# Kernel optimization log

Hardware: AMD Instinct MI355X
Metric: run time of the kernel (lower is better)

Reference implementation:

```python
import jax, jax.numpy as jnp
import numpy as np

B, N, D, E = 2, 50000, 64, 800000


def setup_inputs() -> dict:
    key = jax.random.key(0)
    k = jax.random.split(key, 6)
    return {
        "prev_embeddings": jax.random.normal(k[0], (B, N, D), dtype=jnp.float32),
        "edges_ij": jax.random.randint(k[1], (E, 2), 0, N, dtype=jnp.int64 if jax.config.jax_enable_x64 else jnp.int32),
        "node_features_embeddings": jax.random.normal(k[2], (B, N, D), dtype=jnp.float32),
        "edge_features_embeddings": jax.random.normal(k[3], (B, N, D), dtype=jnp.float32),
        "edge_status": jax.random.uniform(k[4], (E,), dtype=jnp.float32),
        "W": jax.random.normal(k[5], (D, D), dtype=jnp.float32) / np.sqrt(D).astype(np.float32),
    }


def reference(prev_embeddings, edges_ij, node_features_embeddings, edge_features_embeddings, edge_status, W):
    # prev_embeddings: (B, N, D); edges_ij: (E, 2); edge_status: (E,) in [0,1]; W: (D, D) theta2 weight (no bias)
    u = edges_ij[:, 0]
    v = edges_ij[:, 1]
    g = edge_status.astype(prev_embeddings.dtype).reshape(1, -1, 1)  # broadcast (1,E,1) over batch
    h_u = prev_embeddings[:, u, :] * g  # gather source endpoint, gate
    h_v = prev_embeddings[:, v, :] * g  # gather dest endpoint, gate
    # scatter-add gated messages in both directions: nbr[b, v] += h_u, nbr[b, u] += h_v
    nbr = jnp.zeros_like(prev_embeddings).at[:, v, :].add(h_u).at[:, u, :].add(h_v)
    x2 = jnp.einsum('bnd,ed->bne', nbr, W)  # Linear(D,D,bias=False): nbr @ W.T
    return jax.nn.leaky_relu(node_features_embeddings + x2 + edge_features_embeddings)
```

## Files before the change

kernel.cpp:

```cpp
#include <hip/hip_runtime.h>

constexpr int B = 2;
constexpr int N = 50000;
constexpr int D = 64;
constexpr int E = 800000;
constexpr int CAP = 96;
constexpr int XG = 8;
constexpr int NPG = N / XG;
constexpr int CSTRIDE_PAD = 16;

constexpr int ROWS_PER_WAVE = 25;
constexpr int BGROUPS = 1563;
constexpr int PGROUPS = 125;
constexpr int TOTAL_GROUPS = BGROUPS + PGROUPS;

__device__ __forceinline__ unsigned f2bf(float f) {
    unsigned u = __float_as_uint(f);
    return (u + 0x7FFFu + ((u >> 16) & 1u)) >> 16;
}
__device__ __forceinline__ float bfhi2f(unsigned bits) {
    return __uint_as_float(bits & 0xFFFF0000u);
}
__device__ __forceinline__ float bflo2f(unsigned bits) {
    return __uint_as_float(bits << 16);
}

__global__ __launch_bounds__(256) void build_pgemm_fused(
    const int2* __restrict__ edges, const float* __restrict__ status,
    int* __restrict__ counts, unsigned* __restrict__ slots,
    const float* __restrict__ prev, const float* __restrict__ W,
    unsigned* __restrict__ P32, int cstride)
{
    int grp = blockIdx.x >> 3;
    int sub8 = blockIdx.x & 7;
    int t = threadIdx.x;

    int cyc = grp / 13, pos = grp % 13;
    bool is_pgemm = (pos == 12) && (grp < PGROUPS * 13);

    if (!is_pgemm) {
        int b = (grp < PGROUPS * 13) ? (cyc * 12 + pos) : (1500 + (grp - PGROUPS * 13));
        int e0 = b * 512 + t;
        int e1 = e0 + 256;
        bool has1 = (e1 < E);

        int2 uv0 = edges[e0];
        float st0 = status[e0];
        int2 uv1 = has1 ? edges[e1] : uv0;
        float st1 = has1 ? status[e1] : 0.f;
        unsigned gb0 = f2bf(st0) << 16;
        unsigned gb1 = f2bf(st1) << 16;

        bool du0 = (uv0.x / NPG == sub8);
        bool dv0 = (uv0.y / NPG == sub8);
        bool du1 = has1 && (uv1.x / NPG == sub8);
        bool dv1 = has1 && (uv1.y / NPG == sub8);

        int pu0 = CAP, pv0 = CAP, pu1 = CAP, pv1 = CAP;
        if (du0) pu0 = atomicAdd(&counts[(size_t)uv0.x * cstride], 1);
        if (dv0) pv0 = atomicAdd(&counts[(size_t)uv0.y * cstride], 1);
        if (du1) pu1 = atomicAdd(&counts[(size_t)uv1.x * cstride], 1);
        if (dv1) pv1 = atomicAdd(&counts[(size_t)uv1.y * cstride], 1);
        if (du0 && pu0 < CAP) slots[(size_t)uv0.x * CAP + pu0] = gb0 | (unsigned)uv0.y;
        if (dv0 && pv0 < CAP) slots[(size_t)uv0.y * CAP + pv0] = gb0 | (unsigned)uv0.x;
        if (du1 && pu1 < CAP) slots[(size_t)uv1.x * CAP + pu1] = gb1 | (unsigned)uv1.y;
        if (dv1 && pv1 < CAP) slots[(size_t)uv1.y * CAP + pv1] = gb1 | (unsigned)uv1.x;
    } else {
        int pb = cyc * 8 + sub8;
        int wave = t >> 6, lane = t & 63;

        const float4* W4 = (const float4*)W;
        float4 w[16];
#pragma unroll
        for (int q = 0; q < 16; ++q) w[q] = W4[lane * 16 + q];

        int row0 = pb * (4 * ROWS_PER_WAVE) + wave * ROWS_PER_WAVE;
        for (int r = 0; r < ROWS_PER_WAVE; ++r) {
            int row = __builtin_amdgcn_readfirstlane(row0 + r);
            const float* pr = prev + (size_t)row * D;

            float acc = 0.f;
#pragma unroll
            for (int d = 0; d < D; ++d) {
                const float4& wq = w[d >> 2];
                float wd = (d & 3) == 0 ? wq.x : (d & 3) == 1 ? wq.y
                         : (d & 3) == 2 ? wq.z : wq.w;
                acc += pr[d] * wd;
            }

            float partner = __shfl_xor(acc, 1, 64);
            if ((lane & 1) == 0) {
                P32[(size_t)row * 32 + (lane >> 1)] = f2bf(acc) | (f2bf(partner) << 16);
            }
        }
    }
}

__global__ __launch_bounds__(256) void gather_final(
    const uint4* __restrict__ P4,
    const int* __restrict__ counts,
    const unsigned* __restrict__ slots,
    const float* __restrict__ node,
    const float* __restrict__ edgef,
    float* __restrict__ out, int cstride)
{
    __shared__ float xs[4][2][D];

    int t = threadIdx.x;
    int wave = t >> 6, lane = t & 63;
    int n = blockIdx.x * 4 + wave;
    int j = lane & 7;
    int sub = lane >> 3;

    int cnt = min(counts[(size_t)n * cstride], CAP);
    size_t sbase = (size_t)n * CAP;

    float a0[8], a1[8];
#pragma unroll
    for (int i = 0; i < 8; ++i) { a0[i] = 0.f; a1[i] = 0.f; }

    for (int k = sub; k < cnt; k += 8) {
        unsigned ent = slots[sbase + k];
        float g = bfhi2f(ent);
        unsigned nb = ent & 0xFFFFu;
        uint4 r0 = P4[(size_t)nb * 8 + j];
        uint4 r1 = P4[((size_t)N + nb) * 8 + j];
        a0[0] += g * bflo2f(r0.x); a0[1] += g * bfhi2f(r0.x);
        a0[2] += g * bflo2f(r0.y); a0[3] += g * bfhi2f(r0.y);
        a0[4] += g * bflo2f(r0.z); a0[5] += g * bfhi2f(r0.z);
        a0[6] += g * bflo2f(r0.w); a0[7] += g * bfhi2f(r0.w);
        a1[0] += g * bflo2f(r1.x); a1[1] += g * bfhi2f(r1.x);
        a1[2] += g * bflo2f(r1.y); a1[3] += g * bfhi2f(r1.y);
        a1[4] += g * bflo2f(r1.z); a1[5] += g * bfhi2f(r1.z);
        a1[6] += g * bflo2f(r1.w); a1[7] += g * bfhi2f(r1.w);
    }

#pragma unroll
    for (int m = 8; m <= 32; m <<= 1) {
#pragma unroll
        for (int i = 0; i < 8; ++i) {
            a0[i] += __shfl_xor(a0[i], m, 64);
            a1[i] += __shfl_xor(a1[i], m, 64);
        }
    }

    if (sub == 0) {
        *(float4*)&xs[wave][0][j * 8]     = make_float4(a0[0], a0[1], a0[2], a0[3]);
        *(float4*)&xs[wave][0][j * 8 + 4] = make_float4(a0[4], a0[5], a0[6], a0[7]);
        *(float4*)&xs[wave][1][j * 8]     = make_float4(a1[0], a1[1], a1[2], a1[3]);
        *(float4*)&xs[wave][1][j * 8 + 4] = make_float4(a1[4], a1[5], a1[6], a1[7]);
    }
    float s0 = xs[wave][0][lane];
    float s1 = xs[wave][1][lane];

    size_t b0 = (size_t)n * D + lane;
    size_t b1 = (size_t)N * D + b0;
    float y0 = node[b0] + s0 + edgef[b0];
    float y1 = node[b1] + s1 + edgef[b1];
    out[b0] = (y0 >= 0.f) ? y0 : 0.01f * y0;
    out[b1] = (y1 >= 0.f) ? y1 : 0.01f * y1;
}

__device__ inline void atomic_add4(float* p, float4 val, float g) {
    atomicAdd(p + 0, val.x * g);
    atomicAdd(p + 1, val.y * g);
    atomicAdd(p + 2, val.z * g);
    atomicAdd(p + 3, val.w * g);
}

__global__ __launch_bounds__(256) void scatter_kernel(
    const float* __restrict__ prev,
    const int2* __restrict__ edges,
    const float* __restrict__ status,
    float* __restrict__ nbr)
{
    int idx = blockIdx.x * 256 + threadIdx.x;
    int e = idx >> 4;
    int q = idx & 15;
    if (e >= E) return;
    int2 uv = edges[e];
    float g = status[e];
    const float4* p0 = (const float4*)prev;
    const float4* p1 = (const float4*)(prev + (size_t)N * D);
    float4 pu0 = p0[(size_t)uv.x * 16 + q];
    float4 pv0 = p0[(size_t)uv.y * 16 + q];
    float4 pu1 = p1[(size_t)uv.x * 16 + q];
    float4 pv1 = p1[(size_t)uv.y * 16 + q];
    float* n0 = nbr;
    float* n1 = nbr + (size_t)N * D;
    int off_v = uv.y * D + q * 4;
    int off_u = uv.x * D + q * 4;
    atomic_add4(n0 + off_v, pu0, g);
    atomic_add4(n0 + off_u, pv0, g);
    atomic_add4(n1 + off_v, pu1, g);
    atomic_add4(n1 + off_u, pv1, g);
}

__global__ __launch_bounds__(256) void gemm_relu_kernel(
    float* __restrict__ out,
    const float* __restrict__ node,
    const float* __restrict__ edgef,
    const float* __restrict__ W)
{
    __shared__ float Wl[D][D + 1];
    __shared__ float xs[4][D];
    int t = threadIdx.x;
    for (int i = t; i < D * D; i += 256) Wl[i >> 6][i & 63] = W[i];
    int wave = t >> 6, lane = t & 63;
    int row = blockIdx.x * 4 + wave;
    size_t base = (size_t)row * D;
    float x = out[base + lane];
    xs[wave][lane] = x;
    __syncthreads();
    float acc = 0.f;
#pragma unroll
    for (int d = 0; d < D; ++d) acc += xs[wave][d] * Wl[lane][d];
    float y = node[base + lane] + acc + edgef[base + lane];
    out[base + lane] = (y >= 0.f) ? y : 0.01f * y;
}

extern "C" void kernel_launch(void* const* d_in, const int* in_sizes, int n_in,
                              void* d_out, int out_size, void* d_ws, size_t ws_size,
                              hipStream_t stream) {
    const float* prev   = (const float*)d_in[0];
    const int*   edges  = (const int*)d_in[1];
    const float* node   = (const float*)d_in[2];
    const float* edgef  = (const float*)d_in[3];
    const float* status = (const float*)d_in[4];
    const float* W      = (const float*)d_in[5];
    float* out = (float*)d_out;

    const int2* edges2 = (const int2*)edges;

    size_t slots_bytes  = (size_t)N * CAP * sizeof(unsigned);
    size_t p_bytes      = (size_t)B * N * 32 * sizeof(unsigned);
    size_t counts_pad   = (size_t)N * CSTRIDE_PAD * sizeof(int);
    size_t counts_min   = (size_t)N * sizeof(int);

    int cstride;
    size_t counts_bytes;
    if (ws_size >= slots_bytes + counts_pad + p_bytes) {
        cstride = CSTRIDE_PAD; counts_bytes = counts_pad;
    } else if (ws_size >= slots_bytes + counts_min + p_bytes) {
        cstride = 1; counts_bytes = counts_min;
    } else {
        hipMemsetAsync(out, 0, (size_t)B * N * D * sizeof(float), stream);
        scatter_kernel<<<(E * 16) / 256, 256, 0, stream>>>(prev, edges2, status, out);
        gemm_relu_kernel<<<(B * N) / 4, 256, 0, stream>>>(out, node, edgef, W);
        return;
    }

    unsigned* slots = (unsigned*)d_ws;
    int* counts = (int*)((char*)d_ws + slots_bytes);
    unsigned* P32 = (unsigned*)((char*)d_ws + slots_bytes + counts_bytes);

    hipMemsetAsync(counts, 0, counts_bytes, stream);
    build_pgemm_fused<<<TOTAL_GROUPS * 8, 256, 0, stream>>>(
        edges2, status, counts, slots, prev, W, P32, cstride);
    gather_final<<<N / 4, 256, 0, stream>>>(
        (const uint4*)P32, counts, slots, node, edgef, out, cstride);
}
```

Measured before the change: 272.7 us.

## Split projected rows into column-quarter slabs and gather per quarter

The projected bf16 table P is stored as four column-quarter slabs, each interleaved over batch, instead of row-major per node. The gather kernel now makes four passes, each reading a 32-byte piece per neighbor over a smaller slab, so each pass touches a more cache-resident working set. Node and edge-feature loads are hoisted ahead of the gather and use nontemporal loads and stores. The cost is re-reading the slot list four times and doing more shuffle reductions.

```diff
diff --git a/kernel.cpp b/kernel.cpp
--- a/kernel.cpp
+++ b/kernel.cpp
@@ -90,7 +90,9 @@
 
             float partner = __shfl_xor(acc, 1, 64);
             if ((lane & 1) == 0) {
-                P32[(size_t)row * 32 + (lane >> 1)] = f2bf(acc) | (f2bf(partner) << 16);
+                size_t pidx = ((size_t)(lane >> 4) * (B * N) + row) * 8
+                            + ((lane & 15) >> 1);
+                P32[pidx] = f2bf(acc) | (f2bf(partner) << 16);
             }
         }
     }
@@ -109,56 +111,60 @@
     int t = threadIdx.x;
     int wave = t >> 6, lane = t & 63;
     int n = blockIdx.x * 4 + wave;
-    int j = lane & 7;
-    int sub = lane >> 3;
+    int s = lane >> 2;
+    int j = lane & 3;
+    int bb = j >> 1, hf = j & 1;
+
+    size_t b0 = (size_t)n * D + lane;
+    size_t b1 = (size_t)N * D + b0;
+    float nd0 = __builtin_nontemporal_load(node + b0);
+    float ef0 = __builtin_nontemporal_load(edgef + b0);
+    float nd1 = __builtin_nontemporal_load(node + b1);
+    float ef1 = __builtin_nontemporal_load(edgef + b1);
 
     int cnt = min(counts[(size_t)n * cstride], CAP);
     size_t sbase = (size_t)n * CAP;
 
-    float a0[8], a1[8];
-#pragma unroll
-    for (int i = 0; i < 8; ++i) { a0[i] = 0.f; a1[i] = 0.f; }
-
-    for (int k = sub; k < cnt; k += 8) {
-        unsigned ent = slots[sbase + k];
-        float g = bfhi2f(ent);
-        unsigned nb = ent & 0xFFFFu;
-        uint4 r0 = P4[(size_t)nb * 8 + j];
-        uint4 r1 = P4[((size_t)N + nb) * 8 + j];
-        a0[0] += g * bflo2f(r0.x); a0[1] += g * bfhi2f(r0.x);
-        a0[2] += g * bflo2f(r0.y); a0[3] += g * bfhi2f(r0.y);
-        a0[4] += g * bflo2f(r0.z); a0[5] += g * bfhi2f(r0.z);
-        a0[6] += g * bflo2f(r0.w); a0[7] += g * bfhi2f(r0.w);
-        a1[0] += g * bflo2f(r1.x); a1[1] += g * bfhi2f(r1.x);
-        a1[2] += g * bflo2f(r1.y); a1[3] += g * bfhi2f(r1.y);
-        a1[4] += g * bflo2f(r1.z); a1[5] += g * bfhi2f(r1.z);
-        a1[6] += g * bflo2f(r1.w); a1[7] += g * bfhi2f(r1.w);
+#pragma unroll
+    for (int q = 0; q < 4; ++q) {
+        float a[8];
+#pragma unroll
+        for (int i = 0; i < 8; ++i) a[i] = 0.f;
+
+        size_t slab = ((size_t)q * (B * N) + (size_t)bb * N) * 2 + hf;
+
+        for (int k = s; k < cnt; k += 16) {
+            unsigned ent = slots[sbase + k];
+            float g = bfhi2f(ent);
+            unsigned m = ent & 0xFFFFu;
+            uint4 r = P4[slab + (size_t)m * 2];
+            a[0] += g * bflo2f(r.x); a[1] += g * bfhi2f(r.x);
+            a[2] += g * bflo2f(r.y); a[3] += g * bfhi2f(r.y);
+            a[4] += g * bflo2f(r.z); a[5] += g * bfhi2f(r.z);
+            a[6] += g * bflo2f(r.w); a[7] += g * bfhi2f(r.w);
+        }
+
+#pragma unroll
+        for (int mm = 4; mm <= 32; mm <<= 1) {
+#pragma unroll
+            for (int i = 0; i < 8; ++i) a[i] += __shfl_xor(a[i], mm, 64);
+        }
+
+        if (s == 0) {
+            *(float4*)&xs[wave][bb][q * 16 + hf * 8]     = make_float4(a[0], a[1], a[2], a[3]);
+            *(float4*)&xs[wave][bb][q * 16 + hf * 8 + 4] = make_float4(a[4], a[5], a[6], a[7]);
+        }
     }
 
-#pragma unroll
-    for (int m = 8; m <= 32; m <<= 1) {
-#pragma unroll
-        for (int i = 0; i < 8; ++i) {
-            a0[i] += __shfl_xor(a0[i], m, 64);
-            a1[i] += __shfl_xor(a1[i], m, 64);
-        }
-    }
-
-    if (sub == 0) {
-        *(float4*)&xs[wave][0][j * 8]     = make_float4(a0[0], a0[1], a0[2], a0[3]);
-        *(float4*)&xs[wave][0][j * 8 + 4] = make_float4(a0[4], a0[5], a0[6], a0[7]);
-        *(float4*)&xs[wave][1][j * 8]     = make_float4(a1[0], a1[1], a1[2], a1[3]);
-        *(float4*)&xs[wave][1][j * 8 + 4] = make_float4(a1[4], a1[5], a1[6], a1[7]);
-    }
     float s0 = xs[wave][0][lane];
     float s1 = xs[wave][1][lane];
 
-    size_t b0 = (size_t)n * D + lane;
-    size_t b1 = (size_t)N * D + b0;
-    float y0 = node[b0] + s0 + edgef[b0];
-    float y1 = node[b1] + s1 + edgef[b1];
-    out[b0] = (y0 >= 0.f) ? y0 : 0.01f * y0;
-    out[b1] = (y1 >= 0.f) ? y1 : 0.01f * y1;
+    float y0 = nd0 + s0 + ef0;
+    float y1 = nd1 + s1 + ef1;
+    float r0 = (y0 >= 0.f) ? y0 : 0.01f * y0;
+    float r1 = (y1 >= 0.f) ? y1 : 0.01f * y1;
+    __builtin_nontemporal_store(r0, out + b0);
+    __builtin_nontemporal_store(r1, out + b1);
 }
 
 __device__ inline void atomic_add4(float* p, float4 val, float g) {
```

Result: slower. 366.3 us (+34.3%).
